# Performance work log

Hardware: AMD Instinct MI355X
Metric: run time of the kernel (lower is better)

Reference implementation:

```python
import jax, jax.numpy as jnp
import numpy as np

B, S, QD, KVD = 4, 4096, 512, 512  # batch, seq_len (h*w), q_dim, kv_dim
N_HEAD = 1  # original torch view only works for n_head == 1


def setup_inputs() -> dict:
    key = jax.random.key(0)
    ks = jax.random.split(key, 12)
    s_q = 1.0 / np.sqrt(QD)
    s_kv = 1.0 / np.sqrt(KVD)
    return {
        "x": jax.random.normal(ks[0], (B, S, QD), jnp.float32),
        "y": jax.random.normal(ks[1], (B, S, KVD), jnp.float32),
        # torch nn.Linear weights: (out_features, in_features)
        "Wq": jax.random.normal(ks[2], (QD, QD), jnp.float32) * s_q,
        "bq": jnp.zeros((QD,), jnp.float32),
        "Wqv": jax.random.normal(ks[3], (QD, QD), jnp.float32) * s_q,
        "bqv": jnp.zeros((QD,), jnp.float32),
        "Wk": jax.random.normal(ks[4], (QD, KVD), jnp.float32) * s_kv,
        "bk": jnp.zeros((QD,), jnp.float32),
        "Wkv": jax.random.normal(ks[5], (QD, KVD), jnp.float32) * s_kv,
        "bkv": jnp.zeros((QD,), jnp.float32),
        "Wf": jax.random.normal(ks[6], (QD, QD), jnp.float32) * s_q,
        "bf": jnp.zeros((QD,), jnp.float32),
    }


def _linear(t, W, b):
    return jnp.einsum("bsd,od->bso", t, W) + b


def reference(x, y, Wq, bq, Wqv, bqv, Wk, bk, Wkv, bkv, Wf, bf):
    # projections
    q = _linear(x, Wq, bq)     # [B,S,D] query from target face
    qv = _linear(x, Wqv, bqv)  # [B,S,D] additive value stream from query side
    k = _linear(y, Wk, bk)     # [B,S,D]
    kv = _linear(y, Wkv, bkv)  # [B,S,D]
    # n_head == 1: the (B,S,1,D)->(B,1,S,D) transpose is a no-op reshape,
    # so attend directly over [B,S,D]. NOTE: no 1/sqrt(d) scaling (faithful).
    qk = jnp.einsum("bqd,bkd->bqk", q, k)          # [B,S,S]
    attn = jax.nn.softmax(qk, axis=-1)
    out = jnp.einsum("bqk,bkd->bqd", attn, kv) + qv  # fused AV + qv residual
    return _linear(out, Wf, bf)
```

## Files before the change

kernel.cpp:

```cpp
#include <hip/hip_runtime.h>

typedef _Float16 f16;
typedef _Float16 f16x8 __attribute__((ext_vector_type(8)));
typedef _Float16 f16x4 __attribute__((ext_vector_type(4)));
typedef float    f32x4 __attribute__((ext_vector_type(4)));

#define NB 4
#define SEQ 4096
#define DIM 512
#define MTOT (NB*SEQ)
#define NEL ((size_t)MTOT*DIM)

__global__ __launch_bounds__(256) void proj_gemm(
    const float* __restrict__ x, const float* __restrict__ y,
    const float* __restrict__ Wq, const float* __restrict__ bq,
    const float* __restrict__ Wqv, const float* __restrict__ bqv,
    const float* __restrict__ Wk, const float* __restrict__ bk,
    const float* __restrict__ Wkv, const float* __restrict__ bkv,
    f16* __restrict__ qh, f16* __restrict__ qvh,
    f16* __restrict__ kS, f16* __restrict__ vS)
{
    __shared__ __attribute__((aligned(16))) f16 a_lds[128][40];
    __shared__ __attribute__((aligned(16))) f16 b_lds[128][40];

    const int p = blockIdx.z;
    const float* A    = (p < 2) ? x : y;
    const float* W    = (p==0)?Wq:(p==1)?Wqv:(p==2)?Wk:Wkv;
    const float* bias = (p==0)?bq:(p==1)?bqv:(p==2)?bk:bkv;

    const int m0 = blockIdx.y * 128, n0 = blockIdx.x * 128;
    const int tid = threadIdx.x, lane = tid & 63, wv = tid >> 6;
    const int wm = wv >> 1, wn = wv & 1, mrow = lane & 15, qd = lane >> 4;

    f32x4 acc[4][4];
#pragma unroll
    for (int mt = 0; mt < 4; ++mt)
#pragma unroll
        for (int nt = 0; nt < 4; ++nt) acc[mt][nt] = (f32x4){0.f,0.f,0.f,0.f};

    float bv[4];
#pragma unroll
    for (int nt = 0; nt < 4; ++nt) bv[nt] = bias[n0 + wn*64 + nt*16 + mrow];

    for (int k0 = 0; k0 < DIM; k0 += 32) {
        __syncthreads();
#pragma unroll
        for (int i = 0; i < 4; ++i) {
            int c = i*256 + tid;
            int row = c >> 3, c4 = c & 7;
            float4 v = *(const float4*)(A + (size_t)(m0+row)*DIM + k0 + c4*4);
            f16x4 hh = { (f16)v.x, (f16)v.y, (f16)v.z, (f16)v.w };
            *(f16x4*)&a_lds[row][c4*4] = hh;
        }
#pragma unroll
        for (int i = 0; i < 4; ++i) {
            int c = i*256 + tid;
            int row = c >> 3, c4 = c & 7;
            float4 v = *(const float4*)(W + (size_t)(n0+row)*DIM + k0 + c4*4);
            f16x4 hh = { (f16)v.x, (f16)v.y, (f16)v.z, (f16)v.w };
            *(f16x4*)&b_lds[row][c4*4] = hh;
        }
        __syncthreads();
        f16x8 af[4], bfr[4];
#pragma unroll
        for (int mt = 0; mt < 4; ++mt) af[mt]  = *(const f16x8*)&a_lds[wm*64 + mt*16 + mrow][qd*8];
#pragma unroll
        for (int nt = 0; nt < 4; ++nt) bfr[nt] = *(const f16x8*)&b_lds[wn*64 + nt*16 + mrow][qd*8];
#pragma unroll
        for (int mt = 0; mt < 4; ++mt)
#pragma unroll
            for (int nt = 0; nt < 4; ++nt)
                acc[mt][nt] = __builtin_amdgcn_mfma_f32_16x16x32_f16(af[mt], bfr[nt], acc[mt][nt], 0,0,0);
    }

#pragma unroll
    for (int mt = 0; mt < 4; ++mt)
#pragma unroll
        for (int r = 0; r < 4; ++r) {
            int g = m0 + wm*64 + mt*16 + qd*4 + r;
#pragma unroll
            for (int nt = 0; nt < 4; ++nt) {
                int d = n0 + wn*64 + nt*16 + mrow;
                f16 val = (f16)(acc[mt][nt][r] + bv[nt]);
                if (p == 0) {
                    qh[(size_t)g*DIM + d] = val;
                } else if (p == 1) {
                    qvh[(size_t)g*DIM + d] = val;
                } else if (p == 2) {
                    int b = g >> 12, s = g & 4095;
                    int t = s >> 5, n = s & 31;
                    int chunk = d >> 8, ksl = (d >> 5) & 7, q = (d >> 3) & 3, j = d & 7;
                    size_t idx = (((size_t)((b*128 + t)*2048 + chunk*1024
                                   + n*32 + ((ksl*4 + q + n) & 31))) << 3) + j;
                    kS[idx] = val;
                } else {
                    int b = g >> 12, s = g & 4095;
                    int t = s >> 5, q = (s >> 3) & 3, j = s & 7;
                    int chunk = d >> 8, dl = d & 255;
                    size_t idx = (((size_t)((b*128 + t)*2048 + chunk*1024
                                   + dl*4 + ((q + (dl >> 1)) & 3))) << 3) + j;
                    vS[idx] = val;
                }
            }
        }
}

__device__ __forceinline__ void gl_lds16(const f16* g, f16* l)
{
    __builtin_amdgcn_global_load_lds(
        (const __attribute__((address_space(1))) void*)g,
        (__attribute__((address_space(3))) void*)l, 16, 0, 0);
}

__global__ __launch_bounds__(512, 2) void attn_kernel(
    const f16* __restrict__ qh, const f16* __restrict__ kS,
    const f16* __restrict__ vS, const f16* __restrict__ qvh,
    f16* __restrict__ ao)
{
    __shared__ __attribute__((aligned(16))) f16 kbuf[2][16384];
    __shared__ __attribute__((aligned(16))) f16 vbuf[2][16384];
    __shared__ __attribute__((aligned(16))) f16 p_lds[8][16][40];
    __shared__ __attribute__((aligned(16))) f32x4 sx[4][2][2][64];

    const int xcd = blockIdx.x & 7;
    const int b   = xcd >> 1;
    const int qt  = (blockIdx.x >> 3) * 2 + (xcd & 1);
    const int tid = threadIdx.x, lane = tid & 63, w = tid >> 6;
    const int qg = w & 3, h = w >> 2;
    const int mrow = lane & 15, qd = lane >> 4;

    const f16* kSb = kS + ((size_t)b << 21);
    const f16* vSb = vS + ((size_t)b << 21);

    const size_t qrow = ((size_t)b*SEQ + qt*64 + qg*16 + mrow) * DIM;
    f16x8 qf[8];
#pragma unroll
    for (int i = 0; i < 8; ++i)
        qf[i] = *(const f16x8*)(qh + qrow + (h*8 + i)*32 + qd*8);

    f32x4 o[16];
#pragma unroll
    for (int nt = 0; nt < 16; ++nt) o[nt] = (f32x4){0.f,0.f,0.f,0.f};
    f32x4 o_l = (f32x4){0.f,0.f,0.f,0.f};
    float m_i[4] = {-INFINITY,-INFINITY,-INFINITY,-INFINITY};
    const f16x8 ones = {(f16)1.f,(f16)1.f,(f16)1.f,(f16)1.f,
                        (f16)1.f,(f16)1.f,(f16)1.f,(f16)1.f};

#pragma unroll
    for (int u = 0; u < 4; ++u) {
        const int ubase = (u*8 + w) * 64;
        gl_lds16(kSb + (size_t)(ubase + lane)*8, (f16*)&kbuf[0][ubase*8]);
        gl_lds16(vSb + (size_t)(ubase + lane)*8, (f16*)&vbuf[0][ubase*8]);
    }
    __syncthreads();

    const int n0a = mrow, n1a = 16 + mrow;
    const int cbase = h * 1024;

    for (int j = 0; j < 128; ++j) {
        const f16* kb = &kbuf[j & 1][0];
        const f16* vb = &vbuf[j & 1][0];

        if (j < 127) {
            const size_t t0 = (size_t)(j + 1) * 2048;
            f16* kd = &kbuf[(j + 1) & 1][0];
            f16* vd = &vbuf[(j + 1) & 1][0];
#pragma unroll
            for (int u = 0; u < 4; ++u) {
                const int ubase = (u*8 + w) * 64;
                gl_lds16(kSb + (t0 + ubase + lane)*8, kd + ubase*8);
                gl_lds16(vSb + (t0 + ubase + lane)*8, vd + ubase*8);
            }
        }

        f32x4 s0 = (f32x4){0.f,0.f,0.f,0.f}, s1 = s0;
#pragma unroll
        for (int ksl = 0; ksl < 8; ++ksl) {
            f16x8 kf0 = *(const f16x8*)&kb[(cbase + n0a*32 + ((ksl*4 + qd + n0a) & 31)) << 3];
            f16x8 kf1 = *(const f16x8*)&kb[(cbase + n1a*32 + ((ksl*4 + qd + n1a) & 31)) << 3];
            s0 = __builtin_amdgcn_mfma_f32_16x16x32_f16(qf[ksl], kf0, s0, 0,0,0);
            s1 = __builtin_amdgcn_mfma_f32_16x16x32_f16(qf[ksl], kf1, s1, 0,0,0);
        }

        sx[qg][h][0][lane] = s0;
        sx[qg][h][1][lane] = s1;
        __syncthreads();
        {
            f32x4 t0v = sx[qg][h ^ 1][0][lane];
            f32x4 t1v = sx[qg][h ^ 1][1][lane];
#pragma unroll
            for (int rr = 0; rr < 4; ++rr) { s0[rr] += t0v[rr]; s1[rr] += t1v[rr]; }
        }

        float alpha[4];
        bool changed = false;
#pragma unroll
        for (int rr = 0; rr < 4; ++rr) {
            float v = fmaxf(s0[rr], s1[rr]);
            v = fmaxf(v, __shfl_xor(v, 1));
            v = fmaxf(v, __shfl_xor(v, 2));
            v = fmaxf(v, __shfl_xor(v, 4));
            v = fmaxf(v, __shfl_xor(v, 8));
            float mn = fmaxf(m_i[rr], v);
            alpha[rr] = __expf(m_i[rr] - mn);
            if (mn > m_i[rr]) changed = true;
            m_i[rr] = mn;
            s0[rr] = __expf(s0[rr] - mn);
            s1[rr] = __expf(s1[rr] - mn);
        }
        if (__any(changed)) {
#pragma unroll
            for (int nt = 0; nt < 16; ++nt)
#pragma unroll
                for (int rr = 0; rr < 4; ++rr) o[nt][rr] *= alpha[rr];
#pragma unroll
            for (int rr = 0; rr < 4; ++rr) o_l[rr] *= alpha[rr];
        }

#pragma unroll
        for (int rr = 0; rr < 4; ++rr) {
            p_lds[w][qd*4 + rr][mrow]      = (f16)s0[rr];
            p_lds[w][qd*4 + rr][16 + mrow] = (f16)s1[rr];
        }
        f16x8 pf = *(const f16x8*)&p_lds[w][mrow][qd*8];
        o_l = __builtin_amdgcn_mfma_f32_16x16x32_f16(pf, ones, o_l, 0,0,0);

#pragma unroll
        for (int nt = 0; nt < 16; ++nt) {
            int dl = nt*16 + mrow;
            f16x8 vf = *(const f16x8*)&vb[(cbase + dl*4 + ((qd + (dl >> 1)) & 3)) << 3];
            o[nt] = __builtin_amdgcn_mfma_f32_16x16x32_f16(pf, vf, o[nt], 0,0,0);
        }

        __syncthreads();
    }

#pragma unroll
    for (int rr = 0; rr < 4; ++rr) {
        float inv_l = 1.f / o_l[rr];
        size_t grow = ((size_t)b*SEQ + qt*64 + qg*16 + qd*4 + rr) * DIM + h*256;
#pragma unroll
        for (int nt = 0; nt < 16; ++nt) {
            int col = nt*16 + mrow;
            float val = o[nt][rr] * inv_l + (float)qvh[grow + col];
            ao[grow + col] = (f16)val;
        }
    }
}

__global__ __launch_bounds__(256) void final_gemm(
    const f16* __restrict__ ao, const float* __restrict__ Wf,
    const float* __restrict__ bf, float* __restrict__ out)
{
    __shared__ __attribute__((aligned(16))) f16 a_lds[128][40];
    __shared__ __attribute__((aligned(16))) f16 b_lds[128][40];

    const int m0 = blockIdx.y * 128, n0 = blockIdx.x * 128;
    const int tid = threadIdx.x, lane = tid & 63, wv = tid >> 6;
    const int wm = wv >> 1, wn = wv & 1, mrow = lane & 15, qd = lane >> 4;

    f32x4 acc[4][4];
#pragma unroll
    for (int mt = 0; mt < 4; ++mt)
#pragma unroll
        for (int nt = 0; nt < 4; ++nt) acc[mt][nt] = (f32x4){0.f,0.f,0.f,0.f};

    float bv[4];
#pragma unroll
    for (int nt = 0; nt < 4; ++nt) bv[nt] = bf[n0 + wn*64 + nt*16 + mrow];

    for (int k0 = 0; k0 < DIM; k0 += 32) {
        __syncthreads();
#pragma unroll
        for (int i = 0; i < 2; ++i) {
            int c = i*256 + tid;
            int row = c >> 2, c8 = c & 3;
            *(f16x8*)&a_lds[row][c8*8] =
                *(const f16x8*)(ao + (size_t)(m0+row)*DIM + k0 + c8*8);
        }
#pragma unroll
        for (int i = 0; i < 4; ++i) {
            int c = i*256 + tid;
            int row = c >> 3, c4 = c & 7;
            float4 v = *(const float4*)(Wf + (size_t)(n0+row)*DIM + k0 + c4*4);
            f16x4 hh = { (f16)v.x, (f16)v.y, (f16)v.z, (f16)v.w };
            *(f16x4*)&b_lds[row][c4*4] = hh;
        }
        __syncthreads();
        f16x8 af[4], bfr[4];
#pragma unroll
        for (int mt = 0; mt < 4; ++mt) af[mt]  = *(const f16x8*)&a_lds[wm*64 + mt*16 + mrow][qd*8];
#pragma unroll
        for (int nt = 0; nt < 4; ++nt) bfr[nt] = *(const f16x8*)&b_lds[wn*64 + nt*16 + mrow][qd*8];
#pragma unroll
        for (int mt = 0; mt < 4; ++mt)
#pragma unroll
            for (int nt = 0; nt < 4; ++nt)
                acc[mt][nt] = __builtin_amdgcn_mfma_f32_16x16x32_f16(af[mt], bfr[nt], acc[mt][nt], 0,0,0);
    }
#pragma unroll
    for (int mt = 0; mt < 4; ++mt)
#pragma unroll
        for (int r = 0; r < 4; ++r) {
            size_t grow = (size_t)(m0 + wm*64 + mt*16 + qd*4 + r) * DIM;
#pragma unroll
            for (int nt = 0; nt < 4; ++nt) {
                int col = n0 + wn*64 + nt*16 + mrow;
                out[grow + col] = acc[mt][nt][r] + bv[nt];
            }
        }
}

extern "C" void kernel_launch(void* const* d_in, const int* in_sizes, int n_in,
                              void* d_out, int out_size, void* d_ws, size_t ws_size,
                              hipStream_t stream)
{
    const float* x   = (const float*)d_in[0];
    const float* y   = (const float*)d_in[1];
    const float* Wq  = (const float*)d_in[2];
    const float* bq  = (const float*)d_in[3];
    const float* Wqv = (const float*)d_in[4];
    const float* bqv = (const float*)d_in[5];
    const float* Wk  = (const float*)d_in[6];
    const float* bk  = (const float*)d_in[7];
    const float* Wkv = (const float*)d_in[8];
    const float* bkv = (const float*)d_in[9];
    const float* Wf  = (const float*)d_in[10];
    const float* bf  = (const float*)d_in[11];
    float* out = (float*)d_out;

    f16* qh  = (f16*)d_ws;
    f16* qvh = qh  + NEL;
    f16* kS  = qvh + NEL;
    f16* vS  = kS  + NEL;
    f16* aob = vS  + NEL;

    proj_gemm<<<dim3(4, 128, 4), 256, 0, stream>>>(
        x, y, Wq, bq, Wqv, bqv, Wk, bk, Wkv, bkv, qh, qvh, kS, vS);
    attn_kernel<<<dim3(256), 512, 0, stream>>>(qh, kS, vS, qvh, aob);
    final_gemm<<<dim3(4, 128), 256, 0, stream>>>(aob, Wf, bf, out);
}
```

Before: 536.6 us.

## Software-pipeline QK of next tile behind PV and use lazy softmax rescaling

Restructures the attention loop so the QK^T MFMAs for tile j+1 run after the PV MFMAs of tile j. K is prefetched two tiles ahead and V one tile ahead, and the cross-wave score exchange is double-buffered so one barrier per iteration is removed. The online softmax now skips the running-max update unless the new max exceeds the old by more than 8, which avoids most rescales at the cost of a bounded fp16 overflow risk for P. It also reuses the score exchange buffer for the P tile and adds s_setprio hints around the MFMA bursts.

```diff
diff --git a/kernel.cpp b/kernel.cpp
--- a/kernel.cpp
+++ b/kernel.cpp
@@ -119,8 +119,7 @@
 {
     __shared__ __attribute__((aligned(16))) f16 kbuf[2][16384];
     __shared__ __attribute__((aligned(16))) f16 vbuf[2][16384];
-    __shared__ __attribute__((aligned(16))) f16 p_lds[8][16][40];
-    __shared__ __attribute__((aligned(16))) f32x4 sx[4][2][2][64];
+    __shared__ __attribute__((aligned(16))) float xch[2][4][2][512];
 
     const int xcd = blockIdx.x & 7;
     const int b   = xcd >> 1;
@@ -146,54 +145,66 @@
     const f16x8 ones = {(f16)1.f,(f16)1.f,(f16)1.f,(f16)1.f,
                         (f16)1.f,(f16)1.f,(f16)1.f,(f16)1.f};
 
-#pragma unroll
-    for (int u = 0; u < 4; ++u) {
-        const int ubase = (u*8 + w) * 64;
-        gl_lds16(kSb + (size_t)(ubase + lane)*8, (f16*)&kbuf[0][ubase*8]);
-        gl_lds16(vSb + (size_t)(ubase + lane)*8, (f16*)&vbuf[0][ubase*8]);
-    }
-    __syncthreads();
-
     const int n0a = mrow, n1a = 16 + mrow;
     const int cbase = h * 1024;
 
-    for (int j = 0; j < 128; ++j) {
-        const f16* kb = &kbuf[j & 1][0];
-        const f16* vb = &vbuf[j & 1][0];
-
-        if (j < 127) {
-            const size_t t0 = (size_t)(j + 1) * 2048;
-            f16* kd = &kbuf[(j + 1) & 1][0];
-            f16* vd = &vbuf[(j + 1) & 1][0];
-#pragma unroll
-            for (int u = 0; u < 4; ++u) {
-                const int ubase = (u*8 + w) * 64;
-                gl_lds16(kSb + (t0 + ubase + lane)*8, kd + ubase*8);
-                gl_lds16(vSb + (t0 + ubase + lane)*8, vd + ubase*8);
-            }
-        }
-
-        f32x4 s0 = (f32x4){0.f,0.f,0.f,0.f}, s1 = s0;
+#pragma unroll
+    for (int u = 0; u < 4; ++u) {
+        const int ub = (u*8 + w) * 64;
+        gl_lds16(kSb + (size_t)(ub + lane)*8,        (f16*)&kbuf[0][ub*8]);
+    }
+#pragma unroll
+    for (int u = 0; u < 4; ++u) {
+        const int ub = (u*8 + w) * 64;
+        gl_lds16(vSb + (size_t)(ub + lane)*8,        (f16*)&vbuf[0][ub*8]);
+    }
+#pragma unroll
+    for (int u = 0; u < 4; ++u) {
+        const int ub = (u*8 + w) * 64;
+        gl_lds16(kSb + (size_t)(2048 + ub + lane)*8, (f16*)&kbuf[1][ub*8]);
+    }
+    __syncthreads();
+
+    f32x4 s0p = (f32x4){0.f,0.f,0.f,0.f}, s1p = s0p;
+    {
+        const f16* kb = &kbuf[0][0];
+        __builtin_amdgcn_s_setprio(1);
 #pragma unroll
         for (int ksl = 0; ksl < 8; ++ksl) {
             f16x8 kf0 = *(const f16x8*)&kb[(cbase + n0a*32 + ((ksl*4 + qd + n0a) & 31)) << 3];
             f16x8 kf1 = *(const f16x8*)&kb[(cbase + n1a*32 + ((ksl*4 + qd + n1a) & 31)) << 3];
-            s0 = __builtin_amdgcn_mfma_f32_16x16x32_f16(qf[ksl], kf0, s0, 0,0,0);
-            s1 = __builtin_amdgcn_mfma_f32_16x16x32_f16(qf[ksl], kf1, s1, 0,0,0);
-        }
-
-        sx[qg][h][0][lane] = s0;
-        sx[qg][h][1][lane] = s1;
-        __syncthreads();
+            s0p = __builtin_amdgcn_mfma_f32_16x16x32_f16(qf[ksl], kf0, s0p, 0,0,0);
+            s1p = __builtin_amdgcn_mfma_f32_16x16x32_f16(qf[ksl], kf1, s1p, 0,0,0);
+        }
+        __builtin_amdgcn_s_setprio(0);
+        f32x4* slot0 = (f32x4*)&xch[0][qg][h][0];
+        slot0[lane]      = s0p;
+        slot0[64 + lane] = s1p;
+    }
+    __syncthreads();
+
+    for (int j = 0; j < 128; ++j) {
         {
-            f32x4 t0v = sx[qg][h ^ 1][0][lane];
-            f32x4 t1v = sx[qg][h ^ 1][1][lane];
-#pragma unroll
-            for (int rr = 0; rr < 4; ++rr) { s0[rr] += t0v[rr]; s1[rr] += t1v[rr]; }
-        }
-
-        float alpha[4];
-        bool changed = false;
+            const size_t tk = (size_t)((j + 2) & 127) * 2048;
+            const size_t tv = (size_t)((j + 1) & 127) * 2048;
+            f16* kd = &kbuf[j & 1][0];
+            f16* vd = &vbuf[(j + 1) & 1][0];
+#pragma unroll
+            for (int u = 0; u < 4; ++u) {
+                const int ub = (u*8 + w) * 64;
+                gl_lds16(kSb + (tk + ub + lane)*8, kd + ub*8);
+                gl_lds16(vSb + (tv + ub + lane)*8, vd + ub*8);
+            }
+        }
+
+        float* slotr = &xch[j & 1][qg][h ^ 1][0];
+        f32x4 s0 = ((const f32x4*)slotr)[lane];
+        f32x4 s1 = ((const f32x4*)slotr)[64 + lane];
+#pragma unroll
+        for (int rr = 0; rr < 4; ++rr) { s0[rr] += s0p[rr]; s1[rr] += s1p[rr]; }
+
+        float pm[4];
+        bool need = false;
 #pragma unroll
         for (int rr = 0; rr < 4; ++rr) {
             float v = fmaxf(s0[rr], s1[rr]);
@@ -201,35 +212,63 @@
             v = fmaxf(v, __shfl_xor(v, 2));
             v = fmaxf(v, __shfl_xor(v, 4));
             v = fmaxf(v, __shfl_xor(v, 8));
-            float mn = fmaxf(m_i[rr], v);
-            alpha[rr] = __expf(m_i[rr] - mn);
-            if (mn > m_i[rr]) changed = true;
-            m_i[rr] = mn;
-            s0[rr] = __expf(s0[rr] - mn);
-            s1[rr] = __expf(s1[rr] - mn);
-        }
-        if (__any(changed)) {
-#pragma unroll
-            for (int nt = 0; nt < 16; ++nt)
-#pragma unroll
-                for (int rr = 0; rr < 4; ++rr) o[nt][rr] *= alpha[rr];
-#pragma unroll
-            for (int rr = 0; rr < 4; ++rr) o_l[rr] *= alpha[rr];
-        }
-
+            pm[rr] = v;
+            if (v > m_i[rr] + 8.f) need = true;
+        }
+        if (__any(need)) {
+#pragma unroll
+            for (int rr = 0; rr < 4; ++rr) {
+                float mn = fmaxf(m_i[rr], pm[rr]);
+                float alpha = __expf(m_i[rr] - mn);
+                m_i[rr] = mn;
+#pragma unroll
+                for (int nt = 0; nt < 16; ++nt) o[nt][rr] *= alpha;
+                o_l[rr] *= alpha;
+            }
+        }
 #pragma unroll
         for (int rr = 0; rr < 4; ++rr) {
-            p_lds[w][qd*4 + rr][mrow]      = (f16)s0[rr];
-            p_lds[w][qd*4 + rr][16 + mrow] = (f16)s1[rr];
-        }
-        f16x8 pf = *(const f16x8*)&p_lds[w][mrow][qd*8];
+            s0[rr] = __expf(s0[rr] - m_i[rr]);
+            s1[rr] = __expf(s1[rr] - m_i[rr]);
+        }
+
+        f16* pb = (f16*)slotr;
+#pragma unroll
+        for (int rr = 0; rr < 4; ++rr) {
+            pb[(qd*4 + rr)*40 + mrow]      = (f16)s0[rr];
+            pb[(qd*4 + rr)*40 + 16 + mrow] = (f16)s1[rr];
+        }
+        f16x8 pf = *(const f16x8*)&pb[mrow*40 + qd*8];
         o_l = __builtin_amdgcn_mfma_f32_16x16x32_f16(pf, ones, o_l, 0,0,0);
 
-#pragma unroll
-        for (int nt = 0; nt < 16; ++nt) {
-            int dl = nt*16 + mrow;
-            f16x8 vf = *(const f16x8*)&vb[(cbase + dl*4 + ((qd + (dl >> 1)) & 3)) << 3];
-            o[nt] = __builtin_amdgcn_mfma_f32_16x16x32_f16(pf, vf, o[nt], 0,0,0);
+        {
+            const f16* vb = &vbuf[j & 1][0];
+            __builtin_amdgcn_s_setprio(1);
+#pragma unroll
+            for (int nt = 0; nt < 16; ++nt) {
+                int dl = nt*16 + mrow;
+                f16x8 vf = *(const f16x8*)&vb[(cbase + dl*4 + ((qd + (dl >> 1)) & 3)) << 3];
+                o[nt] = __builtin_amdgcn_mfma_f32_16x16x32_f16(pf, vf, o[nt], 0,0,0);
+            }
+            __builtin_amdgcn_s_setprio(0);
+        }
+
+        if (j < 127) {
+            const f16* kb = &kbuf[(j + 1) & 1][0];
+            f32x4 a0 = (f32x4){0.f,0.f,0.f,0.f}, a1 = a0;
+            __builtin_amdgcn_s_setprio(1);
+#pragma unroll
+            for (int ksl = 0; ksl < 8; ++ksl) {
+                f16x8 kf0 = *(const f16x8*)&kb[(cbase + n0a*32 + ((ksl*4 + qd + n0a) & 31)) << 3];
+                f16x8 kf1 = *(const f16x8*)&kb[(cbase + n1a*32 + ((ksl*4 + qd + n1a) & 31)) << 3];
+                a0 = __builtin_amdgcn_mfma_f32_16x16x32_f16(qf[ksl], kf0, a0, 0,0,0);
+                a1 = __builtin_amdgcn_mfma_f32_16x16x32_f16(qf[ksl], kf1, a1, 0,0,0);
+            }
+            __builtin_amdgcn_s_setprio(0);
+            s0p = a0; s1p = a1;
+            f32x4* slotw = (f32x4*)&xch[(j + 1) & 1][qg][h][0];
+            slotw[lane]      = s0p;
+            slotw[64 + lane] = s1p;
         }
 
         __syncthreads();
```

New measurement: 531.4 us. No clear change (-1.0%).
